# Optimization experiments

Hardware: AMD Instinct MI355X
Metric: run time of the kernel (lower is better)

Reference implementation:

```python
import jax, jax.numpy as jnp
import numpy as np

EPS = 1e-5

def _ln(x, g, b):
    mu = jnp.mean(x, axis=-1, keepdims=True)
    var = jnp.mean((x - mu) ** 2, axis=-1, keepdims=True)
    return (x - mu) / jnp.sqrt(var + EPS) * g + b

def setup_inputs() -> dict:
    key = jax.random.key(0)
    ks = jax.random.split(key, 8)
    S, B, L, M, D, Nq, H = 4, 256, 256, 4, 512, 4, 2048
    G = (M + 2) * D
    inp = {
        'ns_tokens': jax.random.normal(ks[0], (B, M, D), jnp.float32),
        'seq_tokens': jax.random.normal(ks[1], (S, B, L, D), jnp.float32),
        'seq_padding_masks': jax.random.randint(ks[2], (S, B, L), 0, 2).astype(bool),
        'seq_stats': jax.random.normal(ks[3], (S, B, 6), jnp.float32),
        'gin_gamma': jnp.ones((G,), jnp.float32),
        'gin_beta': jnp.zeros((G,), jnp.float32),
        'stat_W': 0.02 * jax.random.normal(ks[4], (S, 6, D), jnp.float32),
        'stat_b': jnp.zeros((S, D), jnp.float32),
        'stat_ln_g': jnp.ones((S, D), jnp.float32),
        'stat_ln_b': jnp.zeros((S, D), jnp.float32),
        'W1': 0.02 * jax.random.normal(ks[5], (S, Nq, G, H), jnp.float32),
        'b1': jnp.zeros((S, Nq, H), jnp.float32),
        'W2': 0.02 * jax.random.normal(ks[6], (S, Nq, H, D), jnp.float32),
        'b2': jnp.zeros((S, Nq, D), jnp.float32),
        'ln_g': jnp.ones((S, Nq, D), jnp.float32),
        'ln_b': jnp.zeros((S, Nq, D), jnp.float32),
    }
    return inp

def reference(ns_tokens, seq_tokens, seq_padding_masks, seq_stats,
              gin_gamma, gin_beta, stat_W, stat_b, stat_ln_g, stat_ln_b,
              W1, b1, W2, b2, ln_g, ln_b):
    S, B = seq_tokens.shape[0], ns_tokens.shape[0]
    ns_flat = ns_tokens.reshape(B, -1)                       # (B, M*D)
    valid = (~seq_padding_masks).astype(seq_tokens.dtype)[..., None]  # (S,B,L,1)
    denom = jnp.clip(jnp.sum(valid, axis=2), 1.0)            # (S,B,1)
    pooled = jnp.sum(seq_tokens * valid, axis=2) / denom     # (S,B,D)
    stat = jnp.einsum('sbf,sfd->sbd', seq_stats, stat_W) + stat_b[:, None]
    stat = _ln(stat, stat_ln_g[:, None], stat_ln_b[:, None])  # (S,B,D)
    gi = jnp.concatenate([jnp.broadcast_to(ns_flat[None], (S, B, ns_flat.shape[1])), pooled, stat], axis=-1)
    gi = _ln(gi, gin_gamma, gin_beta)                        # (S,B,G)
    h = jax.nn.silu(jnp.einsum('sbg,sqgh->sqbh', gi, W1) + b1[:, :, None])
    q = jnp.einsum('sqbh,sqhd->sqbd', h, W2) + b2[:, :, None]
    q = _ln(q, ln_g[:, :, None], ln_b[:, :, None])           # (S,Nq,B,D)
    return jnp.transpose(q, (0, 2, 1, 3))                    # (S,B,Nq,D)
```

## Files before the change

kernel.cpp:

```cpp
#include <hip/hip_runtime.h>
#include <hip/hip_bf16.h>

#define S_ 4
#define B_ 256
#define L_ 256
#define D_ 512
#define NQ_ 4
#define H_ 2048
#define G_ 3072

typedef __attribute__((ext_vector_type(4))) float f32x4;
typedef __attribute__((ext_vector_type(8))) short s16x8;

__device__ __forceinline__ unsigned short f2bf(float x) {
    __hip_bfloat16 hb = __float2bfloat16(x);
    return reinterpret_cast<unsigned short&>(hb);
}

__device__ __forceinline__ void gll16(const void* g, void* l) {
    __builtin_amdgcn_global_load_lds(
        (const __attribute__((address_space(1))) unsigned int*)g,
        (__attribute__((address_space(3))) unsigned int*)l, 16, 0, 0);
}

__device__ __forceinline__ float block_sum256(float v, float* red) {
    #pragma unroll
    for (int off = 32; off > 0; off >>= 1) v += __shfl_down(v, off, 64);
    int tid = threadIdx.x;
    int lane = tid & 63, wid = tid >> 6;
    if (lane == 0) red[wid] = v;
    __syncthreads();
    float r = (tid < 4) ? red[tid] : 0.f;
    #pragma unroll
    for (int off = 4; off > 0; off >>= 1) r += __shfl_down(r, off, 64);
    if (tid == 0) red[0] = r;
    __syncthreads();
    float out = red[0];
    __syncthreads();
    return out;
}

__global__ __launch_bounds__(256) void poolgi_kernel(
    const float* __restrict__ seq_tokens,
    const unsigned char* __restrict__ masks_raw,
    const float* __restrict__ ns_tokens,
    const float* __restrict__ seq_stats,
    const float* __restrict__ stat_W,
    const float* __restrict__ stat_b,
    const float* __restrict__ stat_ln_g,
    const float* __restrict__ stat_ln_b,
    const float* __restrict__ gin_gamma,
    const float* __restrict__ gin_beta,
    __hip_bfloat16* __restrict__ gi)
{
    const int sb = blockIdx.x;
    const int s = sb >> 8;
    const int b = sb & 255;
    const int tid = threadIdx.x;

    __shared__ float sval[L_];
    __shared__ float scount[4];
    __shared__ f32x4 spart[256];
    __shared__ float spool[D_];
    __shared__ float sstat[D_];
    __shared__ float red[8];
    __shared__ int is_bool_flag;

    if (tid == 0) is_bool_flag = 0;
    __syncthreads();
    {
        unsigned int w = reinterpret_cast<const unsigned int*>(masks_raw)[tid];
        if (w & 0xFFFFFF00u) is_bool_flag = 1;
    }
    __syncthreads();
    const bool is_bool = (is_bool_flag != 0);

    int mval;
    if (is_bool) mval = masks_raw[(size_t)sb * L_ + tid];
    else         mval = reinterpret_cast<const int*>(masks_raw)[(size_t)sb * L_ + tid];
    float valid = mval ? 0.f : 1.f;
    sval[tid] = valid;
    float c = valid;
    #pragma unroll
    for (int off = 32; off > 0; off >>= 1) c += __shfl_down(c, off, 64);
    if ((tid & 63) == 0) scount[tid >> 6] = c;
    __syncthreads();
    const float denom = fmaxf(scount[0] + scount[1] + scount[2] + scount[3], 1.f);

    const float* base = seq_tokens + (size_t)sb * L_ * D_;
    const int cidx = tid & 127;
    const int rg = tid >> 7;
    f32x4 acc = {0.f, 0.f, 0.f, 0.f};
    for (int l = rg; l < L_; l += 2) {
        float vl = sval[l];
        f32x4 v = *reinterpret_cast<const f32x4*>(base + (size_t)l * D_ + cidx * 4);
        acc += v * vl;
    }
    spart[tid] = acc;
    __syncthreads();
    if (tid < 128) {
        f32x4 r = spart[tid] + spart[tid + 128];
        r *= (1.f / denom);
        *reinterpret_cast<f32x4*>(&spool[cidx * 4]) = r;
    }
    __syncthreads();

    float st[6];
    #pragma unroll
    for (int f = 0; f < 6; ++f) st[f] = seq_stats[(size_t)sb * 6 + f];

    float sp[2];
    #pragma unroll
    for (int k = 0; k < 2; ++k) {
        int d = tid + k * 256;
        float a = stat_b[s * D_ + d];
        #pragma unroll
        for (int f = 0; f < 6; ++f) a += st[f] * stat_W[(s * 6 + f) * D_ + d];
        sp[k] = a;
    }
    float ssum = block_sum256(sp[0] + sp[1], red);
    float ssq  = block_sum256(sp[0] * sp[0] + sp[1] * sp[1], red);
    float mu = ssum / D_;
    float var = ssq / D_ - mu * mu;
    float rinv = rsqrtf(var + 1e-5f);
    #pragma unroll
    for (int k = 0; k < 2; ++k) {
        int d = tid + k * 256;
        sstat[d] = (sp[k] - mu) * rinv * stat_ln_g[s * D_ + d] + stat_ln_b[s * D_ + d];
    }
    __syncthreads();

    float gv[12];
    float gsum = 0.f, gsq = 0.f;
    #pragma unroll
    for (int k = 0; k < 12; ++k) {
        int g = tid + k * 256;
        float v;
        if (g < 2048)       v = ns_tokens[(size_t)b * 2048 + g];
        else if (g < 2560)  v = spool[g - 2048];
        else                v = sstat[g - 2560];
        gv[k] = v;
        gsum += v;
        gsq += v * v;
    }
    gsum = block_sum256(gsum, red);
    gsq  = block_sum256(gsq, red);
    mu = gsum / G_;
    var = gsq / G_ - mu * mu;
    rinv = rsqrtf(var + 1e-5f);
    #pragma unroll
    for (int k = 0; k < 12; ++k) {
        int g = tid + k * 256;
        float o = (gv[k] - mu) * rinv * gin_gamma[g] + gin_beta[g];
        gi[(size_t)sb * G_ + g] = __float2bfloat16(o);
    }
}

__global__ __launch_bounds__(256) void gemm1_kernel(
    const __hip_bfloat16* __restrict__ gi,
    const float* __restrict__ W1,
    const float* __restrict__ b1,
    __hip_bfloat16* __restrict__ hbuf)
{
    const int bid = blockIdx.x;
    const int wg = (bid & 7) * 64 + (bid >> 3);
    const int ntile = wg & 31;
    const int sq = wg >> 5;
    const int s = sq >> 2;
    const int tid = threadIdx.x;
    const int lane = tid & 63;
    const int wid = tid >> 6;

    __shared__ __align__(16) unsigned short As[2][256 * 64];
    __shared__ __align__(16) unsigned short Ws[2][64 * 64];

    const __hip_bfloat16* Ab = gi + (size_t)s * B_ * G_;
    const float* Wb = W1 + (size_t)sq * G_ * H_ + ntile * 64;

    f32x4 acc[4][4];
    #pragma unroll
    for (int i = 0; i < 4; ++i)
        #pragma unroll
        for (int j = 0; j < 4; ++j) acc[i][j] = (f32x4){0.f, 0.f, 0.f, 0.f};

    const __hip_bfloat16* aptr[8];
    #pragma unroll
    for (int i = 0; i < 8; ++i) {
        int row = wid * 64 + i * 8 + (lane >> 3);
        int swz = ((lane >> 3) ^ i) & 7;
        aptr[i] = Ab + (size_t)row * G_ + (((lane & 7) ^ swz) * 8);
    }

    const int wn0 = (tid & 15) * 4;
    const int wk0 = (tid >> 4) * 4;
    int offW[4];
    #pragma unroll
    for (int nn = 0; nn < 4; ++nn) {
        int row = wn0 + nn;
        int swz = (row ^ (row >> 3)) & 7;
        offW[nn] = (row * 128 + wk0 * 2) ^ (swz << 4);
    }

    int offA[2][4], offB[2][4];
    #pragma unroll
    for (int kb = 0; kb < 2; ++kb) {
        #pragma unroll
        for (int mi = 0; mi < 4; ++mi) {
            int r = wid * 64 + mi * 16 + (lane & 15);
            int swz = (r ^ (r >> 3)) & 7;
            offA[kb][mi] = r * 128 + ((((lane >> 4) + kb * 4) ^ swz) * 16);
        }
        #pragma unroll
        for (int ni = 0; ni < 4; ++ni) {
            int r = ni * 16 + (lane & 15);
            int swz = (r ^ (r >> 3)) & 7;
            offB[kb][ni] = r * 128 + ((((lane >> 4) + kb * 4) ^ swz) * 16);
        }
    }

    {
        #pragma unroll
        for (int i = 0; i < 8; ++i)
            gll16(aptr[i], &As[0][(wid * 64 + i * 8) * 64]);
        const float* wp = Wb + (size_t)wk0 * H_ + wn0;
        f32x4 w0[4];
        #pragma unroll
        for (int kk = 0; kk < 4; ++kk)
            w0[kk] = *reinterpret_cast<const f32x4*>(wp + (size_t)kk * H_);
        #pragma unroll
        for (int nn = 0; nn < 4; ++nn) {
            unsigned long long pk =
                (unsigned long long)f2bf(w0[0][nn]) |
                ((unsigned long long)f2bf(w0[1][nn]) << 16) |
                ((unsigned long long)f2bf(w0[2][nn]) << 32) |
                ((unsigned long long)f2bf(w0[3][nn]) << 48);
            *reinterpret_cast<unsigned long long*>(reinterpret_cast<char*>(&Ws[0][0]) + offW[nn]) = pk;
        }
        __syncthreads();
    }

    for (int kt = 0; kt < G_ / 64; ++kt) {
        const int cur = kt & 1, nxt = cur ^ 1;
        const bool pf = (kt < G_ / 64 - 1);
        f32x4 wv[4];
        if (pf) {
            const int kb2 = (kt + 1) * 64;
            #pragma unroll
            for (int i = 0; i < 8; ++i)
                gll16(aptr[i] + kb2, &As[nxt][(wid * 64 + i * 8) * 64]);
            const float* wp = Wb + (size_t)(kb2 + wk0) * H_ + wn0;
            #pragma unroll
            for (int kk = 0; kk < 4; ++kk)
                wv[kk] = *reinterpret_cast<const f32x4*>(wp + (size_t)kk * H_);
        }

        const char* Al = reinterpret_cast<const char*>(&As[cur][0]);
        const char* Wl = reinterpret_cast<const char*>(&Ws[cur][0]);
        #pragma unroll
        for (int kb = 0; kb < 2; ++kb) {
            s16x8 af[4], bfr[4];
            #pragma unroll
            for (int mi = 0; mi < 4; ++mi)
                af[mi] = *reinterpret_cast<const s16x8*>(Al + offA[kb][mi]);
            #pragma unroll
            for (int ni = 0; ni < 4; ++ni)
                bfr[ni] = *reinterpret_cast<const s16x8*>(Wl + offB[kb][ni]);
            #pragma unroll
            for (int mi = 0; mi < 4; ++mi)
                #pragma unroll
                for (int ni = 0; ni < 4; ++ni)
                    acc[mi][ni] = __builtin_amdgcn_mfma_f32_16x16x32_bf16(af[mi], bfr[ni], acc[mi][ni], 0, 0, 0);
        }

        if (pf) {
            #pragma unroll
            for (int nn = 0; nn < 4; ++nn) {
                unsigned long long pk =
                    (unsigned long long)f2bf(wv[0][nn]) |
                    ((unsigned long long)f2bf(wv[1][nn]) << 16) |
                    ((unsigned long long)f2bf(wv[2][nn]) << 32) |
                    ((unsigned long long)f2bf(wv[3][nn]) << 48);
                *reinterpret_cast<unsigned long long*>(reinterpret_cast<char*>(&Ws[nxt][0]) + offW[nn]) = pk;
            }
        }
        __syncthreads();
    }

    const float* b1p = b1 + (size_t)sq * H_ + ntile * 64;
    __hip_bfloat16* hp = hbuf + (size_t)sq * B_ * H_;
    #pragma unroll
    for (int mi = 0; mi < 4; ++mi)
        #pragma unroll
        for (int ni = 0; ni < 4; ++ni)
            #pragma unroll
            for (int r = 0; r < 4; ++r) {
                int row = wid * 64 + mi * 16 + ((lane >> 4) << 2) + r;
                int coll = ni * 16 + (lane & 15);
                float x = acc[mi][ni][r] + b1p[coll];
                float sg = 1.f / (1.f + __expf(-x));
                hp[(size_t)row * H_ + ntile * 64 + coll] = __float2bfloat16(x * sg);
            }
}

__global__ __launch_bounds__(256) void gemm2_kernel(
    const __hip_bfloat16* __restrict__ hbuf,
    const float* __restrict__ W2,
    float* __restrict__ qpre)
{
    const int ntile = blockIdx.x;
    const int mtile = blockIdx.y;
    const int sq = blockIdx.z;
    const int tid = threadIdx.x;
    const int lane = tid & 63;
    const int wid = tid >> 6;
    const int wm = wid >> 1, wn = wid & 1;

    __shared__ __align__(16) unsigned short As[128 * 64];
    __shared__ __align__(16) unsigned short Ws[64 * 64];

    const __hip_bfloat16* Ab = hbuf + ((size_t)sq * B_ + mtile * 128) * H_;
    const float* Wb = W2 + (size_t)sq * H_ * D_ + ntile * 64;

    f32x4 acc[4][2];
    #pragma unroll
    for (int i = 0; i < 4; ++i)
        #pragma unroll
        for (int j = 0; j < 2; ++j) acc[i][j] = (f32x4){0.f, 0.f, 0.f, 0.f};

    const int wn0 = (tid & 15) * 4;
    const int wk0 = (tid >> 4) * 4;

    for (int kt = 0; kt < H_ / 64; ++kt) {
        const int kbase = kt * 64;
        __syncthreads();
        #pragma unroll
        for (int i = 0; i < 4; ++i) {
            int slot = i * 256 + tid;
            int row = slot >> 3, cc = slot & 7;
            int swz = (row ^ (row >> 3)) & 7;
            s16x8 v = *reinterpret_cast<const s16x8*>(Ab + (size_t)row * H_ + kbase + cc * 8);
            *reinterpret_cast<s16x8*>(&As[row * 64 + ((cc ^ swz) * 8)]) = v;
        }
        float wv[4][4];
        #pragma unroll
        for (int kk = 0; kk < 4; ++kk) {
            f32x4 t = *reinterpret_cast<const f32x4*>(Wb + (size_t)(kbase + wk0 + kk) * D_ + wn0);
            #pragma unroll
            for (int j = 0; j < 4; ++j) wv[kk][j] = t[j];
        }
        #pragma unroll
        for (int nn = 0; nn < 4; ++nn) {
            int row = wn0 + nn;
            int swz = (row ^ (row >> 3)) & 7;
            unsigned long long pk =
                (unsigned long long)f2bf(wv[0][nn]) |
                ((unsigned long long)f2bf(wv[1][nn]) << 16) |
                ((unsigned long long)f2bf(wv[2][nn]) << 32) |
                ((unsigned long long)f2bf(wv[3][nn]) << 48);
            int byteoff = (row * 128 + wk0 * 2) ^ (swz << 4);
            *reinterpret_cast<unsigned long long*>(reinterpret_cast<char*>(Ws) + byteoff) = pk;
        }
        __syncthreads();
        #pragma unroll
        for (int kb = 0; kb < 2; ++kb) {
            s16x8 af[4], bfr[2];
            #pragma unroll
            for (int mi = 0; mi < 4; ++mi) {
                int r = wm * 64 + mi * 16 + (lane & 15);
                int swz = (r ^ (r >> 3)) & 7;
                int chunk = ((lane >> 4) + kb * 4) ^ swz;
                af[mi] = *reinterpret_cast<const s16x8*>(&As[r * 64 + chunk * 8]);
            }
            #pragma unroll
            for (int ni = 0; ni < 2; ++ni) {
                int r = wn * 32 + ni * 16 + (lane & 15);
                int swz = (r ^ (r >> 3)) & 7;
                int chunk = ((lane >> 4) + kb * 4) ^ swz;
                bfr[ni] = *reinterpret_cast<const s16x8*>(&Ws[r * 64 + chunk * 8]);
            }
            #pragma unroll
            for (int mi = 0; mi < 4; ++mi)
                #pragma unroll
                for (int ni = 0; ni < 2; ++ni)
                    acc[mi][ni] = __builtin_amdgcn_mfma_f32_16x16x32_bf16(af[mi], bfr[ni], acc[mi][ni], 0, 0, 0);
        }
    }
    #pragma unroll
    for (int mi = 0; mi < 4; ++mi)
        #pragma unroll
        for (int ni = 0; ni < 2; ++ni)
            #pragma unroll
            for (int r = 0; r < 4; ++r) {
                int row = mtile * 128 + wm * 64 + mi * 16 + ((lane >> 4) << 2) + r;
                int col = ntile * 64 + wn * 32 + ni * 16 + (lane & 15);
                qpre[((size_t)sq * B_ + row) * D_ + col] = acc[mi][ni][r];
            }
}

__global__ __launch_bounds__(256) void lnout_kernel(
    const float* __restrict__ qpre,
    const float* __restrict__ b2,
    const float* __restrict__ lng,
    const float* __restrict__ lnb,
    float* __restrict__ out)
{
    const int idx = blockIdx.x;
    const int sq = idx >> 8;
    const int b = idx & 255;
    const int tid = threadIdx.x;
    __shared__ float red[8];

    float v[2];
    #pragma unroll
    for (int k = 0; k < 2; ++k) {
        int d = tid + k * 256;
        v[k] = qpre[(size_t)idx * D_ + d] + b2[sq * D_ + d];
    }
    float sum = block_sum256(v[0] + v[1], red);
    float sq2 = block_sum256(v[0] * v[0] + v[1] * v[1], red);
    float mu = sum / D_;
    float var = sq2 / D_ - mu * mu;
    float rinv = rsqrtf(var + 1e-5f);
    const int s = sq >> 2, q = sq & 3;
    #pragma unroll
    for (int k = 0; k < 2; ++k) {
        int d = tid + k * 256;
        float o = (v[k] - mu) * rinv * lng[sq * D_ + d] + lnb[sq * D_ + d];
        out[(((size_t)s * B_ + b) * NQ_ + q) * D_ + d] = o;
    }
}

extern "C" void kernel_launch(void* const* d_in, const int* in_sizes, int n_in,
                              void* d_out, int out_size, void* d_ws, size_t ws_size,
                              hipStream_t stream) {
    const float* ns_tokens   = (const float*)d_in[0];
    const float* seq_tokens  = (const float*)d_in[1];
    const unsigned char* masks = (const unsigned char*)d_in[2];
    const float* seq_stats   = (const float*)d_in[3];
    const float* gin_gamma   = (const float*)d_in[4];
    const float* gin_beta    = (const float*)d_in[5];
    const float* stat_W      = (const float*)d_in[6];
    const float* stat_b      = (const float*)d_in[7];
    const float* stat_ln_g   = (const float*)d_in[8];
    const float* stat_ln_b   = (const float*)d_in[9];
    const float* W1          = (const float*)d_in[10];
    const float* b1          = (const float*)d_in[11];
    const float* W2          = (const float*)d_in[12];
    const float* b2          = (const float*)d_in[13];
    const float* ln_g        = (const float*)d_in[14];
    const float* ln_b        = (const float*)d_in[15];
    float* out = (float*)d_out;

    char* ws = (char*)d_ws;
    __hip_bfloat16* gi   = (__hip_bfloat16*)(ws);
    __hip_bfloat16* hbuf = (__hip_bfloat16*)(ws + 6291456);
    float* qpre          = (float*)(ws + 6291456 + 16777216);

    poolgi_kernel<<<dim3(S_ * B_), dim3(256), 0, stream>>>(
        seq_tokens, masks, ns_tokens, seq_stats, stat_W, stat_b,
        stat_ln_g, stat_ln_b, gin_gamma, gin_beta, gi);
    gemm1_kernel<<<dim3(32 * S_ * NQ_), dim3(256), 0, stream>>>(gi, W1, b1, hbuf);
    gemm2_kernel<<<dim3(D_ / 64, B_ / 128, S_ * NQ_), dim3(256), 0, stream>>>(hbuf, W2, qpre);
    lnout_kernel<<<dim3(S_ * NQ_ * B_), dim3(256), 0, stream>>>(qpre, b2, ln_g, ln_b, out);
}
```

Before: 288.7 us.

## Narrow gemm1 N-tile, single-buffer LDS for occupancy, store qpre as bf16

gemm1 now uses 32-column N tiles instead of 64, which doubles the grid to 1024 blocks. It drops LDS double buffering so each block uses about 36KB instead of about 80KB, and adds launch bounds targeting 4 blocks per CU, trading in-block prefetch overlap for overlap across waves from more resident blocks. W1 is register-prefetched one tile ahead, but A now loads synchronously with two barriers per k-step. gemm2 writes its intermediate as bf16 rather than fp32 to halve that traffic, at some precision cost before the final layernorm.

```diff
diff --git a/kernel.cpp b/kernel.cpp
--- a/kernel.cpp
+++ b/kernel.cpp
@@ -156,52 +156,52 @@
     }
 }
 
-__global__ __launch_bounds__(256) void gemm1_kernel(
+__global__ __launch_bounds__(256, 4) void gemm1_kernel(
     const __hip_bfloat16* __restrict__ gi,
     const float* __restrict__ W1,
     const float* __restrict__ b1,
     __hip_bfloat16* __restrict__ hbuf)
 {
     const int bid = blockIdx.x;
-    const int wg = (bid & 7) * 64 + (bid >> 3);
-    const int ntile = wg & 31;
-    const int sq = wg >> 5;
+    const int wg = (bid & 7) * 128 + (bid >> 3);
+    const int ntile = wg & 63;
+    const int sq = wg >> 6;
     const int s = sq >> 2;
     const int tid = threadIdx.x;
     const int lane = tid & 63;
     const int wid = tid >> 6;
 
-    __shared__ __align__(16) unsigned short As[2][256 * 64];
-    __shared__ __align__(16) unsigned short Ws[2][64 * 64];
-
-    const __hip_bfloat16* Ab = gi + (size_t)s * B_ * G_;
-    const float* Wb = W1 + (size_t)sq * G_ * H_ + ntile * 64;
-
-    f32x4 acc[4][4];
+    __shared__ __align__(16) unsigned short As[256 * 64];
+    __shared__ __align__(16) unsigned short Ws[32 * 64];
+
+    const char* Ag = reinterpret_cast<const char*>(gi + (size_t)s * B_ * G_);
+    const float* Wb = W1 + (size_t)sq * G_ * H_ + ntile * 32;
+
+    f32x4 acc[4][2];
     #pragma unroll
     for (int i = 0; i < 4; ++i)
         #pragma unroll
-        for (int j = 0; j < 4; ++j) acc[i][j] = (f32x4){0.f, 0.f, 0.f, 0.f};
-
-    const __hip_bfloat16* aptr[8];
+        for (int j = 0; j < 2; ++j) acc[i][j] = (f32x4){0.f, 0.f, 0.f, 0.f};
+
+    unsigned aoff[8];
     #pragma unroll
     for (int i = 0; i < 8; ++i) {
         int row = wid * 64 + i * 8 + (lane >> 3);
         int swz = ((lane >> 3) ^ i) & 7;
-        aptr[i] = Ab + (size_t)row * G_ + (((lane & 7) ^ swz) * 8);
-    }
-
-    const int wn0 = (tid & 15) * 4;
-    const int wk0 = (tid >> 4) * 4;
-    int offW[4];
+        aoff[i] = (unsigned)row * (G_ * 2) + (((lane & 7) ^ swz) * 16);
+    }
+
+    const int wn0 = (tid & 7) * 4;
+    const int wk0 = (tid >> 3) * 2;
+    unsigned offW[4];
     #pragma unroll
     for (int nn = 0; nn < 4; ++nn) {
         int row = wn0 + nn;
         int swz = (row ^ (row >> 3)) & 7;
-        offW[nn] = (row * 128 + wk0 * 2) ^ (swz << 4);
-    }
-
-    int offA[2][4], offB[2][4];
+        offW[nn] = (unsigned)((row * 128 + wk0 * 2) ^ (swz << 4));
+    }
+
+    unsigned offA[2][4], offB[2][2];
     #pragma unroll
     for (int kb = 0; kb < 2; ++kb) {
         #pragma unroll
@@ -211,101 +211,84 @@
             offA[kb][mi] = r * 128 + ((((lane >> 4) + kb * 4) ^ swz) * 16);
         }
         #pragma unroll
-        for (int ni = 0; ni < 4; ++ni) {
+        for (int ni = 0; ni < 2; ++ni) {
             int r = ni * 16 + (lane & 15);
             int swz = (r ^ (r >> 3)) & 7;
             offB[kb][ni] = r * 128 + ((((lane >> 4) + kb * 4) ^ swz) * 16);
         }
     }
 
-    {
-        #pragma unroll
-        for (int i = 0; i < 8; ++i)
-            gll16(aptr[i], &As[0][(wid * 64 + i * 8) * 64]);
-        const float* wp = Wb + (size_t)wk0 * H_ + wn0;
-        f32x4 w0[4];
-        #pragma unroll
-        for (int kk = 0; kk < 4; ++kk)
-            w0[kk] = *reinterpret_cast<const f32x4*>(wp + (size_t)kk * H_);
-        #pragma unroll
-        for (int nn = 0; nn < 4; ++nn) {
-            unsigned long long pk =
-                (unsigned long long)f2bf(w0[0][nn]) |
-                ((unsigned long long)f2bf(w0[1][nn]) << 16) |
-                ((unsigned long long)f2bf(w0[2][nn]) << 32) |
-                ((unsigned long long)f2bf(w0[3][nn]) << 48);
-            *reinterpret_cast<unsigned long long*>(reinterpret_cast<char*>(&Ws[0][0]) + offW[nn]) = pk;
-        }
+    char* AsU = reinterpret_cast<char*>(As);
+    #pragma unroll
+    for (int i = 0; i < 8; ++i)
+        gll16(Ag + aoff[i], AsU + (wid * 64 + i * 8) * 128);
+    f32x4 wreg[2];
+    #pragma unroll
+    for (int kk = 0; kk < 2; ++kk)
+        wreg[kk] = *reinterpret_cast<const f32x4*>(Wb + (size_t)(wk0 + kk) * H_ + wn0);
+
+    for (int kt = 0; kt < G_ / 64; ++kt) {
+        unsigned pk[4];
+        #pragma unroll
+        for (int nn = 0; nn < 4; ++nn)
+            pk[nn] = (unsigned)f2bf(wreg[0][nn]) | ((unsigned)f2bf(wreg[1][nn]) << 16);
+
         __syncthreads();
-    }
-
-    for (int kt = 0; kt < G_ / 64; ++kt) {
-        const int cur = kt & 1, nxt = cur ^ 1;
-        const bool pf = (kt < G_ / 64 - 1);
-        f32x4 wv[4];
-        if (pf) {
-            const int kb2 = (kt + 1) * 64;
+        #pragma unroll
+        for (int nn = 0; nn < 4; ++nn)
+            *reinterpret_cast<unsigned*>(reinterpret_cast<char*>(Ws) + offW[nn]) = pk[nn];
+        if (kt > 0) {
+            const unsigned kbyte = (unsigned)kt * 128;
             #pragma unroll
             for (int i = 0; i < 8; ++i)
-                gll16(aptr[i] + kb2, &As[nxt][(wid * 64 + i * 8) * 64]);
-            const float* wp = Wb + (size_t)(kb2 + wk0) * H_ + wn0;
-            #pragma unroll
-            for (int kk = 0; kk < 4; ++kk)
-                wv[kk] = *reinterpret_cast<const f32x4*>(wp + (size_t)kk * H_);
-        }
-
-        const char* Al = reinterpret_cast<const char*>(&As[cur][0]);
-        const char* Wl = reinterpret_cast<const char*>(&Ws[cur][0]);
+                gll16(Ag + (aoff[i] + kbyte), AsU + (wid * 64 + i * 8) * 128);
+        }
+        __syncthreads();
+
+        if (kt < G_ / 64 - 1) {
+            const float* wp = Wb + (size_t)((kt + 1) * 64 + wk0) * H_ + wn0;
+            #pragma unroll
+            for (int kk = 0; kk < 2; ++kk)
+                wreg[kk] = *reinterpret_cast<const f32x4*>(wp + (size_t)kk * H_);
+        }
+
+        const char* Al = reinterpret_cast<const char*>(As);
+        const char* Wl = reinterpret_cast<const char*>(Ws);
         #pragma unroll
         for (int kb = 0; kb < 2; ++kb) {
-            s16x8 af[4], bfr[4];
-            #pragma unroll
-            for (int mi = 0; mi < 4; ++mi)
-                af[mi] = *reinterpret_cast<const s16x8*>(Al + offA[kb][mi]);
-            #pragma unroll
-            for (int ni = 0; ni < 4; ++ni)
+            s16x8 bfr[2];
+            #pragma unroll
+            for (int ni = 0; ni < 2; ++ni)
                 bfr[ni] = *reinterpret_cast<const s16x8*>(Wl + offB[kb][ni]);
             #pragma unroll
-            for (int mi = 0; mi < 4; ++mi)
-                #pragma unroll
-                for (int ni = 0; ni < 4; ++ni)
-                    acc[mi][ni] = __builtin_amdgcn_mfma_f32_16x16x32_bf16(af[mi], bfr[ni], acc[mi][ni], 0, 0, 0);
-        }
-
-        if (pf) {
-            #pragma unroll
-            for (int nn = 0; nn < 4; ++nn) {
-                unsigned long long pk =
-                    (unsigned long long)f2bf(wv[0][nn]) |
-                    ((unsigned long long)f2bf(wv[1][nn]) << 16) |
-                    ((unsigned long long)f2bf(wv[2][nn]) << 32) |
-                    ((unsigned long long)f2bf(wv[3][nn]) << 48);
-                *reinterpret_cast<unsigned long long*>(reinterpret_cast<char*>(&Ws[nxt][0]) + offW[nn]) = pk;
+            for (int mi = 0; mi < 4; ++mi) {
+                s16x8 af = *reinterpret_cast<const s16x8*>(Al + offA[kb][mi]);
+                acc[mi][0] = __builtin_amdgcn_mfma_f32_16x16x32_bf16(af, bfr[0], acc[mi][0], 0, 0, 0);
+                acc[mi][1] = __builtin_amdgcn_mfma_f32_16x16x32_bf16(af, bfr[1], acc[mi][1], 0, 0, 0);
             }
         }
-        __syncthreads();
-    }
-
-    const float* b1p = b1 + (size_t)sq * H_ + ntile * 64;
+    }
+
+    const float* b1p = b1 + (size_t)sq * H_ + ntile * 32;
     __hip_bfloat16* hp = hbuf + (size_t)sq * B_ * H_;
     #pragma unroll
     for (int mi = 0; mi < 4; ++mi)
         #pragma unroll
-        for (int ni = 0; ni < 4; ++ni)
+        for (int ni = 0; ni < 2; ++ni)
             #pragma unroll
             for (int r = 0; r < 4; ++r) {
                 int row = wid * 64 + mi * 16 + ((lane >> 4) << 2) + r;
                 int coll = ni * 16 + (lane & 15);
                 float x = acc[mi][ni][r] + b1p[coll];
                 float sg = 1.f / (1.f + __expf(-x));
-                hp[(size_t)row * H_ + ntile * 64 + coll] = __float2bfloat16(x * sg);
+                hp[(size_t)row * H_ + ntile * 32 + coll] = __float2bfloat16(x * sg);
             }
 }
 
 __global__ __launch_bounds__(256) void gemm2_kernel(
     const __hip_bfloat16* __restrict__ hbuf,
     const float* __restrict__ W2,
-    float* __restrict__ qpre)
+    __hip_bfloat16* __restrict__ qpre)
 {
     const int ntile = blockIdx.x;
     const int mtile = blockIdx.y;
@@ -393,12 +376,12 @@
             for (int r = 0; r < 4; ++r) {
                 int row = mtile * 128 + wm * 64 + mi * 16 + ((lane >> 4) << 2) + r;
                 int col = ntile * 64 + wn * 32 + ni * 16 + (lane & 15);
-                qpre[((size_t)sq * B_ + row) * D_ + col] = acc[mi][ni][r];
+                qpre[((size_t)sq * B_ + row) * D_ + col] = __float2bfloat16(acc[mi][ni][r]);
             }
 }
 
 __global__ __launch_bounds__(256) void lnout_kernel(
-    const float* __restrict__ qpre,
+    const __hip_bfloat16* __restrict__ qpre,
     const float* __restrict__ b2,
     const float* __restrict__ lng,
     const float* __restrict__ lnb,
@@ -414,7 +397,7 @@
     #pragma unroll
     for (int k = 0; k < 2; ++k) {
         int d = tid + k * 256;
-        v[k] = qpre[(size_t)idx * D_ + d] + b2[sq * D_ + d];
+        v[k] = __bfloat162float(qpre[(size_t)idx * D_ + d]) + b2[sq * D_ + d];
     }
     float sum = block_sum256(v[0] + v[1], red);
     float sq2 = block_sum256(v[0] * v[0] + v[1] * v[1], red);
@@ -454,12 +437,12 @@
     char* ws = (char*)d_ws;
     __hip_bfloat16* gi   = (__hip_bfloat16*)(ws);
     __hip_bfloat16* hbuf = (__hip_bfloat16*)(ws + 6291456);
-    float* qpre          = (float*)(ws + 6291456 + 16777216);
+    __hip_bfloat16* qpre = (__hip_bfloat16*)(ws + 6291456 + 16777216);
 
     poolgi_kernel<<<dim3(S_ * B_), dim3(256), 0, stream>>>(
         seq_tokens, masks, ns_tokens, seq_stats, stat_W, stat_b,
         stat_ln_g, stat_ln_b, gin_gamma, gin_beta, gi);
-    gemm1_kernel<<<dim3(32 * S_ * NQ_), dim3(256), 0, stream>>>(gi, W1, b1, hbuf);
+    gemm1_kernel<<<dim3(64 * S_ * NQ_), dim3(256), 0, stream>>>(gi, W1, b1, hbuf);
     gemm2_kernel<<<dim3(D_ / 64, B_ / 128, S_ * NQ_), dim3(256), 0, stream>>>(hbuf, W2, qpre);
     lnout_kernel<<<dim3(S_ * NQ_ * B_), dim3(256), 0, stream>>>(qpre, b2, ln_g, ln_b, out);
 }
```

Measured after the change: 296.4 us. 1.03x slower.
